# Kernel optimization log

Measured on AMD Instinct MI355X. Metric: run time of the kernel, lower is better.

Reference implementation:

```python
import jax, jax.numpy as jnp
import numpy as np

B, H, W = 32, 512, 1024


def setup_inputs() -> dict:
    key = jax.random.key(0)
    k1, k2, k3 = jax.random.split(key, 3)
    depth = jax.random.uniform(k1, (B, 1, H, W), dtype=jnp.float32)
    inv_K = jax.random.normal(k2, (B, 4, 4), dtype=jnp.float32)
    dxy = jax.random.randint(k3, (B, 2), 0, 100, dtype=jnp.int32)
    return {"depth": depth, "inv_K": inv_K, "dxy": dxy}


def reference(depth, inv_K, dxy):
    # Base pixel grid, xy-indexed meshgrid flattened row-major: [2, H*W]
    xs = jnp.arange(W, dtype=jnp.float32)
    ys = jnp.arange(H, dtype=jnp.float32)
    gx, gy = jnp.meshgrid(xs, ys, indexing="xy")  # each [H, W]
    base = jnp.stack([gx.ravel(), gy.ravel()], axis=0)  # [2, H*W]
    # Per-sample offset: pix[b] = base + dxy[b, :, None]  -> [B, 2, H*W]
    pix = base[None, :, :] + dxy.astype(jnp.float32)[:, :, None]
    ones = jnp.ones((B, 1, H * W), dtype=depth.dtype)
    pix_h = jnp.concatenate([pix, ones], axis=1)  # [B, 3, H*W]
    # cam = inv_K[:, :3, :3] @ pix_h, scaled by depth
    cam = jnp.einsum("bij,bjn->bin", inv_K[:, :3, :3], pix_h)  # [B, 3, H*W]
    cam = depth.reshape(B, 1, H * W) * cam
    return jnp.concatenate([cam, ones], axis=1)  # [B, 4, H*W]
```

## Files before the change

### kernel.cpp

```cpp
#include <hip/hip_runtime.h>


#define BB 32
#define HH 512
#define WW 1024
#define HWN (HH * WW)

typedef float vf4 __attribute__((ext_vector_type(4)));

__global__ __launch_bounds__(256) void backproject_kernel(
    const float* __restrict__ depth,
    const float* __restrict__ invK,
    const int*   __restrict__ dxy,
    float*       __restrict__ out)
{
    const int tid  = threadIdx.x;
    const int b    = blockIdx.y;
    const int row0 = blockIdx.x * 2;
    const int xpix = tid * 4;
    const int n0   = row0 * WW + xpix;

    const float k00 = invK[b * 16 + 0];
    const float k01 = invK[b * 16 + 1];
    const float k02 = invK[b * 16 + 2];
    const float k10 = invK[b * 16 + 4];
    const float k11 = invK[b * 16 + 5];
    const float k12 = invK[b * 16 + 6];
    const float k20 = invK[b * 16 + 8];
    const float k21 = invK[b * 16 + 9];
    const float k22 = invK[b * 16 + 10];
    const float dx  = (float)dxy[b * 2 + 0];
    const float dy  = (float)dxy[b * 2 + 1];

    const float x0 = (float)xpix + dx;

    const float* dbase = depth + (size_t)b * HWN + n0;
    const vf4 da = *(const vf4*)(dbase);
    const vf4 db = *(const vf4*)(dbase + WW);

    float* outb = out + (size_t)b * 4 * HWN;
    const vf4 ones = {1.f, 1.f, 1.f, 1.f};

    #pragma unroll
    for (int h = 0; h < 2; ++h) {
        const vf4   d = h ? db : da;
        const float y = (float)(row0 + h) + dy;
        const float c0 = k01 * y + k02;
        const float c1 = k11 * y + k12;
        const float c2 = k21 * y + k22;

        vf4 r0, r1, r2;
        r0.x = d.x * (k00 * (x0 + 0.f) + c0);
        r0.y = d.y * (k00 * (x0 + 1.f) + c0);
        r0.z = d.z * (k00 * (x0 + 2.f) + c0);
        r0.w = d.w * (k00 * (x0 + 3.f) + c0);

        r1.x = d.x * (k10 * (x0 + 0.f) + c1);
        r1.y = d.y * (k10 * (x0 + 1.f) + c1);
        r1.z = d.z * (k10 * (x0 + 2.f) + c1);
        r1.w = d.w * (k10 * (x0 + 3.f) + c1);

        r2.x = d.x * (k20 * (x0 + 0.f) + c2);
        r2.y = d.y * (k20 * (x0 + 1.f) + c2);
        r2.z = d.z * (k20 * (x0 + 2.f) + c2);
        r2.w = d.w * (k20 * (x0 + 3.f) + c2);

        const int n = n0 + h * WW;
        *(vf4*)(outb + 0 * HWN + n) = r0;
        *(vf4*)(outb + 1 * HWN + n) = r1;
        *(vf4*)(outb + 2 * HWN + n) = r2;
        *(vf4*)(outb + 3 * HWN + n) = ones;
    }
}

extern "C" void kernel_launch(void* const* d_in, const int* in_sizes, int n_in,
                              void* d_out, int out_size, void* d_ws, size_t ws_size,
                              hipStream_t stream) {
    const float* depth = (const float*)d_in[0];
    const float* invK  = (const float*)d_in[1];
    const int*   dxy   = (const int*)d_in[2];
    float*       out   = (float*)d_out;

    dim3 grid(HH / 2, BB);
    backproject_kernel<<<grid, 256, 0, stream>>>(depth, invK, dxy, out);
}
```

Baseline: 314.3 us.

## Remap threads to one output channel each and loop over batches

The grid becomes 1D, with 2048 blocks. Each thread owns one 4-pixel vector of one output channel (c = 0..3) and loops over all 32 batches, loading only that channel's invK row, now wave-uniform via readfirstlane. Threads on channel 3 only write ones, so that branch is uniform per block. In exchange, the depth input is now read three times (once per channel c = 0..2) instead of once. Fewer, longer-running threads also change how much memory-level parallelism the kernel can sustain.

```diff
diff --git a/kernel.cpp b/kernel.cpp
--- a/kernel.cpp
+++ b/kernel.cpp
@@ -14,62 +14,48 @@
     const int*   __restrict__ dxy,
     float*       __restrict__ out)
 {
-    const int tid  = threadIdx.x;
-    const int b    = blockIdx.y;
-    const int row0 = blockIdx.x * 2;
-    const int xpix = tid * 4;
-    const int n0   = row0 * WW + xpix;
+    const int gid = blockIdx.x * 256 + threadIdx.x;
+    const int o   = gid * 4;
+    const int c   = o >> 19;
+    const int n   = o & (HWN - 1);
+    const float xf = (float)(n & (WW - 1));
+    const float yf = (float)(n >> 10);
 
-    const float k00 = invK[b * 16 + 0];
-    const float k01 = invK[b * 16 + 1];
-    const float k02 = invK[b * 16 + 2];
-    const float k10 = invK[b * 16 + 4];
-    const float k11 = invK[b * 16 + 5];
-    const float k12 = invK[b * 16 + 6];
-    const float k20 = invK[b * 16 + 8];
-    const float k21 = invK[b * 16 + 9];
-    const float k22 = invK[b * 16 + 10];
-    const float dx  = (float)dxy[b * 2 + 0];
-    const float dy  = (float)dxy[b * 2 + 1];
-
-    const float x0 = (float)xpix + dx;
-
-    const float* dbase = depth + (size_t)b * HWN + n0;
-    const vf4 da = *(const vf4*)(dbase);
-    const vf4 db = *(const vf4*)(dbase + WW);
-
-    float* outb = out + (size_t)b * 4 * HWN;
     const vf4 ones = {1.f, 1.f, 1.f, 1.f};
 
-    #pragma unroll
-    for (int h = 0; h < 2; ++h) {
-        const vf4   d = h ? db : da;
-        const float y = (float)(row0 + h) + dy;
-        const float c0 = k01 * y + k02;
-        const float c1 = k11 * y + k12;
-        const float c2 = k21 * y + k22;
+    if (c == 3) {
+        float* optr = out + o;
+        #pragma unroll 4
+        for (int b = 0; b < BB; ++b, optr += 4 * HWN)
+            *(vf4*)optr = ones;
+        return;
+    }
 
-        vf4 r0, r1, r2;
-        r0.x = d.x * (k00 * (x0 + 0.f) + c0);
-        r0.y = d.y * (k00 * (x0 + 1.f) + c0);
-        r0.z = d.z * (k00 * (x0 + 2.f) + c0);
-        r0.w = d.w * (k00 * (x0 + 3.f) + c0);
+    const int cs = __builtin_amdgcn_readfirstlane(c);
 
-        r1.x = d.x * (k10 * (x0 + 0.f) + c1);
-        r1.y = d.y * (k10 * (x0 + 1.f) + c1);
-        r1.z = d.z * (k10 * (x0 + 2.f) + c1);
-        r1.w = d.w * (k10 * (x0 + 3.f) + c1);
+    const float* dptr = depth + n;
+    float*       optr = out + o;
 
-        r2.x = d.x * (k20 * (x0 + 0.f) + c2);
-        r2.y = d.y * (k20 * (x0 + 1.f) + c2);
-        r2.z = d.z * (k20 * (x0 + 2.f) + c2);
-        r2.w = d.w * (k20 * (x0 + 3.f) + c2);
+    #pragma unroll 2
+    for (int b = 0; b < BB; ++b, dptr += HWN, optr += 4 * HWN) {
+        const float a0 = invK[b * 16 + cs * 4 + 0];
+        const float a1 = invK[b * 16 + cs * 4 + 1];
+        const float a2 = invK[b * 16 + cs * 4 + 2];
+        const float dx = (float)dxy[b * 2 + 0];
+        const float dy = (float)dxy[b * 2 + 1];
 
-        const int n = n0 + h * WW;
-        *(vf4*)(outb + 0 * HWN + n) = r0;
-        *(vf4*)(outb + 1 * HWN + n) = r1;
-        *(vf4*)(outb + 2 * HWN + n) = r2;
-        *(vf4*)(outb + 3 * HWN + n) = ones;
+        const float x0 = xf + dx;
+        const float cc = __builtin_fmaf(a1, yf + dy, a2);
+
+        const vf4 d = *(const vf4*)dptr;
+
+        vf4 r;
+        r.x = d.x * __builtin_fmaf(a0, x0 + 0.f, cc);
+        r.y = d.y * __builtin_fmaf(a0, x0 + 1.f, cc);
+        r.z = d.z * __builtin_fmaf(a0, x0 + 2.f, cc);
+        r.w = d.w * __builtin_fmaf(a0, x0 + 3.f, cc);
+
+        *(vf4*)optr = r;
     }
 }
 
@@ -81,6 +67,5 @@
     const int*   dxy   = (const int*)d_in[2];
     float*       out   = (float*)d_out;
 
-    dim3 grid(HH / 2, BB);
-    backproject_kernel<<<grid, 256, 0, stream>>>(depth, invK, dxy, out);
+    backproject_kernel<<<dim3(2048), 256, 0, stream>>>(depth, invK, dxy, out);
 }
```

Result: no change. 318.4 us (+1.3%).
